# Performance work log

Measured on AMD Instinct MI355X. Metric: run time of the kernel, lower is better.

## Reference

```python
import jax, jax.numpy as jnp
import numpy as np
from jax import lax

B, C_IN, OUT_C, FEAT, W, HEADS, EXP = 2, 3, 12, 1024, 512, 4, 4
HEAD_DIM = FEAT // HEADS
EPS = 1e-8


def _u(key, shape, bound):
    return jax.random.uniform(key, shape, jnp.float32, -bound, bound)


def setup_inputs():
    key = jax.random.key(0)
    ks = jax.random.split(key, 16)
    fb = 1.0 / np.sqrt(FEAT)
    return {
        'x': jax.random.normal(ks[0], (B, C_IN, FEAT, W), jnp.float32),
        'embed_w': _u(ks[1], (OUT_C, C_IN, 1, 1), 1.0 / np.sqrt(C_IN)),
        'embed_b': _u(ks[2], (OUT_C,), 1.0 / np.sqrt(C_IN)),
        'ln1_w': jnp.ones((OUT_C, 1, FEAT), jnp.float32),
        'ln1_b': jnp.zeros((OUT_C, 1, FEAT), jnp.float32),
        'q_dw': _u(ks[3], (OUT_C, 1, 9, 9), 1.0 / 9.0),
        'q_pw': _u(ks[4], (OUT_C, FEAT, FEAT), fb),
        'k_dw': _u(ks[5], (OUT_C, 1, 9, 9), 1.0 / 9.0),
        'k_pw': _u(ks[6], (OUT_C, FEAT, FEAT), fb),
        'v_dw': _u(ks[7], (OUT_C, 1, 9, 9), 1.0 / 9.0),
        'v_pw': _u(ks[8], (OUT_C, FEAT, FEAT), fb),
        'o_pw': _u(ks[9], (OUT_C, FEAT, FEAT), fb),
        'ln2_w': jnp.ones((OUT_C, 1, FEAT), jnp.float32),
        'ln2_b': jnp.zeros((OUT_C, 1, FEAT), jnp.float32),
        'c1_w': _u(ks[10], (OUT_C * EXP, OUT_C, 3, 3), 1.0 / np.sqrt(OUT_C * 9)),
        'c1_b': _u(ks[11], (OUT_C * EXP,), 1.0 / np.sqrt(OUT_C * 9)),
        'c2_w': _u(ks[12], (OUT_C, OUT_C * EXP, 3, 3), 1.0 / np.sqrt(OUT_C * EXP * 9)),
        'c2_b': _u(ks[13], (OUT_C,), 1.0 / np.sqrt(OUT_C * EXP * 9)),
    }


def conv2d(x, w, b=None, pad=1, groups=1):
    y = lax.conv_general_dilated(x, w, (1, 1), [(pad, pad), (pad, pad)],
                                 dimension_numbers=('NCHW', 'OIHW', 'NCHW'),
                                 feature_group_count=groups)
    if b is not None:
        y = y + b[None, :, None, None]
    return y


def mc_layernorm(x, w, b):
    # LayerNorm over the feature (H) axis, per-channel affine. x: (b,c,h,w)
    xt = jnp.swapaxes(x, 2, 3)  # b,c,w,h
    mu = xt.mean(-1, keepdims=True)
    var = xt.var(-1, keepdims=True)
    y = (xt - mu) / jnp.sqrt(var + EPS) * w[:, 0, :][None, :, None, :] + b[:, 0, :][None, :, None, :]
    return jnp.swapaxes(y, 2, 3)


def mc_linear(x, w_pw):
    # per-channel linear over feature axis. x: (b,c,h,w), w_pw: (c,out_f,in_f)
    return jnp.einsum('bchw,cfh->bcfw', x, w_pw)


def rope(x):
    # interleaved rotary along the frame axis. x: (b,c,heads,w,d)
    d = x.shape[-1]
    inv = 1.0 / (10000.0 ** (jnp.arange(0, d, 2, dtype=jnp.float32) / d))
    t = jnp.arange(x.shape[-2], dtype=jnp.float32)
    freqs = jnp.repeat(t[:, None] * inv[None, :], 2, axis=-1)  # (w, d)
    cos, sin = jnp.cos(freqs), jnp.sin(freqs)
    xp = x.reshape(x.shape[:-1] + (d // 2, 2))
    xr = jnp.stack([-xp[..., 1], xp[..., 0]], -1).reshape(x.shape)
    return x * cos + xr * sin


def attention(x, q_dw, q_pw, k_dw, k_pw, v_dw, v_pw, o_pw):
    b, c, h, w = x.shape

    def proj(dw, pw):
        y = mc_linear(conv2d(x, dw, pad=4, groups=c), pw)  # b,c,h,w
        return jnp.swapaxes(y, 2, 3).reshape(b, c, w, HEADS, HEAD_DIM).transpose(0, 1, 3, 2, 4)

    q = rope(proj(q_dw, q_pw))
    k = rope(proj(k_dw, k_pw))
    v = proj(v_dw, v_pw)
    # NOTE: original scales by sqrt(h) = sqrt(features), not sqrt(head_dim)
    qk = jnp.einsum('bcnqd,bcnkd->bcnqk', q, k) / jnp.sqrt(jnp.float32(h))
    a = jnp.einsum('bcnqk,bcnkd->bcnqd', jax.nn.softmax(qk, -1), v)
    a = a.transpose(0, 1, 3, 2, 4).reshape(b, c, w, h)
    a = jnp.swapaxes(a, 2, 3)  # b,c,h,w
    return mc_linear(a, o_pw), qk


def _forward(x, embed_w, embed_b, ln1_w, ln1_b, q_dw, q_pw, k_dw, k_pw, v_dw, v_pw,
             o_pw, ln2_w, ln2_b, c1_w, c1_b, c2_w, c2_b):
    h = conv2d(x, embed_w, embed_b, pad=0)
    z, qk = attention(mc_layernorm(h, ln1_w, ln1_b), q_dw, q_pw, k_dw, k_pw, v_dw, v_pw, o_pw)
    h = h + z
    t = conv2d(mc_layernorm(h, ln2_w, ln2_b), c1_w, c1_b, pad=1)
    t = jnp.square(jax.nn.relu(t))
    z = conv2d(t, c2_w, c2_b, pad=1)
    h = h + z
    return jnp.concatenate((x, h), axis=1), h, qk


def reference(x, embed_w, embed_b, ln1_w, ln1_b, q_dw, q_pw, k_dw, k_pw, v_dw, v_pw,
              o_pw, ln2_w, ln2_b, c1_w, c1_b, c2_w, c2_b):
    return _forward(x, embed_w, embed_b, ln1_w, ln1_b, q_dw, q_pw, k_dw, k_pw, v_dw,
                    v_pw, o_pw, ln2_w, ln2_b, c1_w, c1_b, c2_w, c2_b)
```

## Files before the change

kernel.cpp:

```cpp
#include <hip/hip_runtime.h>
#include <math.h>

static constexpr int FEAT = 1024;
static constexpr int WDIM = 512;
static constexpr size_t PL = (size_t)FEAT * WDIM;
static constexpr size_t NB = (size_t)2 * 12 * PL;
static constexpr size_t HS = NB / 2;

typedef __attribute__((ext_vector_type(8))) short bf8_t;
typedef __attribute__((ext_vector_type(4))) float f4_t;

__device__ __forceinline__ ushort f2b(float f) {
  union { float f; unsigned u; } x; x.f = f;
  unsigned u = x.u;
  return (ushort)((u + 0x7FFFu + ((u >> 16) & 1u)) >> 16);
}

#define GLL16(g, l) __builtin_amdgcn_global_load_lds(                         \
    (const __attribute__((address_space(1))) void*)(g),                       \
    (__attribute__((address_space(3))) void*)(l), 16, 0, 0)

__global__ __launch_bounds__(256)
void k_embed(const float* __restrict__ x, const float* __restrict__ ew,
             const float* __restrict__ eb, float* __restrict__ h0)
{
  int t = blockIdx.x * 256 + threadIdx.x;
  int x4 = (t & 127) * 4;
  int y  = (t >> 7) & 1023;
  int b  = t >> 17;
  float4 xi0 = *(const float4*)&x[(((size_t)b*3+0)*FEAT + y)*WDIM + x4];
  float4 xi1 = *(const float4*)&x[(((size_t)b*3+1)*FEAT + y)*WDIM + x4];
  float4 xi2 = *(const float4*)&x[(((size_t)b*3+2)*FEAT + y)*WDIM + x4];
  #pragma unroll
  for (int c = 0; c < 12; c++) {
    float w0 = ew[c*3], w1 = ew[c*3+1], w2 = ew[c*3+2], bb = eb[c];
    float4 o;
    o.x = fmaf(xi0.x, w0, fmaf(xi1.x, w1, fmaf(xi2.x, w2, bb)));
    o.y = fmaf(xi0.y, w0, fmaf(xi1.y, w1, fmaf(xi2.y, w2, bb)));
    o.z = fmaf(xi0.z, w0, fmaf(xi1.z, w1, fmaf(xi2.z, w2, bb)));
    o.w = fmaf(xi0.w, w0, fmaf(xi1.w, w1, fmaf(xi2.w, w2, bb)));
    *(float4*)&h0[(((size_t)b*12+c)*FEAT + y)*WDIM + x4] = o;
  }
}

__global__ __launch_bounds__(256)
void k_ln(const float* __restrict__ in, const float* __restrict__ w,
          const float* __restrict__ bia, float* __restrict__ out)
{
  int bc = blockIdx.y; int c = bc % 12;
  int w0 = blockIdx.x * 64;
  int tx = threadIdx.x & 63, ty = threadIdx.x >> 6;
  const float* base = in + (size_t)bc*PL + w0;
  float s = 0.f, ss = 0.f;
  for (int h = ty; h < FEAT; h += 4) {
    float v = base[(size_t)h*WDIM + tx];
    s += v; ss = fmaf(v, v, ss);
  }
  __shared__ float S1[4][64], S2[4][64];
  S1[ty][tx] = s; S2[ty][tx] = ss;
  __syncthreads();
  if (ty == 0) {
    float t1 = S1[0][tx]+S1[1][tx]+S1[2][tx]+S1[3][tx];
    float t2 = S2[0][tx]+S2[1][tx]+S2[2][tx]+S2[3][tx];
    float mu = t1 * (1.0f/1024.0f);
    float var = t2 * (1.0f/1024.0f) - mu*mu;
    S1[0][tx] = mu; S2[0][tx] = rsqrtf(var + 1e-8f);
  }
  __syncthreads();
  float mu = S1[0][tx], ri = S2[0][tx];
  float* ob = out + (size_t)bc*PL + w0;
  for (int h = ty; h < FEAT; h += 4) {
    float v = base[(size_t)h*WDIM + tx];
    ob[(size_t)h*WDIM + tx] = (v - mu) * ri * w[c*FEAT + h] + bia[c*FEAT + h];
  }
}

__global__ __launch_bounds__(256)
void k_ln_b(const float* __restrict__ in, const float* __restrict__ w,
            const float* __restrict__ bia, ushort* __restrict__ out)
{
  int bc = blockIdx.y; int c = bc % 12;
  int w0 = blockIdx.x * 64;
  int tx = threadIdx.x & 63, ty = threadIdx.x >> 6;
  const float* base = in + (size_t)bc*PL + w0;
  float s = 0.f, ss = 0.f;
  for (int h = ty; h < FEAT; h += 4) {
    float v = base[(size_t)h*WDIM + tx];
    s += v; ss = fmaf(v, v, ss);
  }
  __shared__ float S1[4][64], S2[4][64];
  S1[ty][tx] = s; S2[ty][tx] = ss;
  __syncthreads();
  if (ty == 0) {
    float t1 = S1[0][tx]+S1[1][tx]+S1[2][tx]+S1[3][tx];
    float t2 = S2[0][tx]+S2[1][tx]+S2[2][tx]+S2[3][tx];
    float mu = t1 * (1.0f/1024.0f);
    float var = t2 * (1.0f/1024.0f) - mu*mu;
    S1[0][tx] = mu; S2[0][tx] = rsqrtf(var + 1e-8f);
  }
  __syncthreads();
  float mu = S1[0][tx], ri = S2[0][tx];
  ushort* ob = out + (size_t)bc*PL + w0;
  for (int h = ty; h < FEAT; h += 4) {
    float v = base[(size_t)h*WDIM + tx];
    ob[(size_t)h*WDIM + tx] = f2b((v - mu) * ri * w[c*FEAT + h] + bia[c*FEAT + h]);
  }
}

__global__ __launch_bounds__(256)
void k_dw3(const float* __restrict__ in, const float* __restrict__ wq,
           const float* __restrict__ wk, const float* __restrict__ wv,
           float* __restrict__ oq, float* __restrict__ ok, float* __restrict__ ov)
{
  __shared__ float tile[12][72];
  __shared__ float wsq[81], wsk[81], wsv[81];
  int bc = blockIdx.z; int c = bc % 12;
  int y0 = blockIdx.y * 4, w0 = blockIdx.x * 64;
  int tid = threadIdx.x;
  const float* base = in + (size_t)bc*PL;
  for (int idx = tid; idx < 12*72; idx += 256) {
    int hh = idx / 72, ww = idx % 72;
    int gh = y0 + hh - 4, gw = w0 + ww - 4;
    float v = 0.f;
    if (gh >= 0 && gh < 1024 && gw >= 0 && gw < 512) v = base[(size_t)gh*WDIM + gw];
    tile[hh][ww] = v;
  }
  if (tid < 81) { wsq[tid] = wq[c*81+tid]; wsk[tid] = wk[c*81+tid]; wsv[tid] = wv[c*81+tid]; }
  __syncthreads();
  int tx = tid & 63, ty = tid >> 6;
  float aq = 0.f, ak = 0.f, av = 0.f;
  #pragma unroll
  for (int dy = 0; dy < 9; dy++)
    #pragma unroll
    for (int dx = 0; dx < 9; dx++) {
      float v = tile[ty+dy][tx+dx];
      aq = fmaf(v, wsq[dy*9+dx], aq);
      ak = fmaf(v, wsk[dy*9+dx], ak);
      av = fmaf(v, wsv[dy*9+dx], av);
    }
  size_t o = (size_t)bc*PL + (size_t)(y0+ty)*WDIM + (w0+tx);
  oq[o] = aq; ok[o] = ak; ov[o] = av;
}

__global__ __launch_bounds__(256)
void k_tr3(const float* __restrict__ iq, const float* __restrict__ ik,
           const float* __restrict__ iv, ushort* __restrict__ oq,
           ushort* __restrict__ ok, ushort* __restrict__ ov)
{
  __shared__ float t[64][65];
  int bc = blockIdx.z; int h0 = blockIdx.y * 64, w0 = blockIdx.x * 64;
  size_t ib = (size_t)bc * PL;
  const float* ins[3] = {iq + ib, ik + ib, iv + ib};
  ushort* outs[3] = {oq + ib, ok + ib, ov + ib};
  #pragma unroll
  for (int a = 0; a < 3; a++) {
    if (a) __syncthreads();
    for (int i = threadIdx.x; i < 4096; i += 256) {
      int hh = i >> 6, ww = i & 63;
      t[hh][ww] = ins[a][(size_t)(h0+hh)*512 + w0 + ww];
    }
    __syncthreads();
    for (int i = threadIdx.x; i < 4096; i += 256) {
      int ww = i >> 6, hh = i & 63;
      outs[a][(size_t)(w0+ww)*1024 + h0 + hh] = f2b(t[hh][ww]);
    }
  }
}

__global__ __launch_bounds__(256)
void k_cvt(const float* __restrict__ in, ushort* __restrict__ out)
{
  size_t i = ((size_t)blockIdx.x * 256 + threadIdx.x) * 8;
  float4 v0 = *(const float4*)&in[i];
  float4 v1 = *(const float4*)&in[i+4];
  union { ushort u[8]; uint4 v; } o;
  o.u[0]=f2b(v0.x); o.u[1]=f2b(v0.y); o.u[2]=f2b(v0.z); o.u[3]=f2b(v0.w);
  o.u[4]=f2b(v1.x); o.u[5]=f2b(v1.y); o.u[6]=f2b(v1.z); o.u[7]=f2b(v1.w);
  *(uint4*)&out[i] = o.v;
}

__global__ __launch_bounds__(256)
void k_softmax(const float* __restrict__ qk, ushort* __restrict__ probs)
{
  int wave = threadIdx.x >> 6, lane = threadIdx.x & 63;
  size_t row = (size_t)blockIdx.x * 4 + wave;
  const float* r = qk + row * 512;
  float v[8];
  float m = -1e30f;
  #pragma unroll
  for (int j = 0; j < 8; j++) { v[j] = r[lane + 64*j]; m = fmaxf(m, v[j]); }
  #pragma unroll
  for (int o = 32; o; o >>= 1) m = fmaxf(m, __shfl_xor(m, o));
  float s = 0.f;
  #pragma unroll
  for (int j = 0; j < 8; j++) { v[j] = expf(v[j] - m); s += v[j]; }
  #pragma unroll
  for (int o = 32; o; o >>= 1) s += __shfl_xor(s, o);
  float inv = 1.0f / s;
  ushort* p = probs + row * 512;
  #pragma unroll
  for (int j = 0; j < 8; j++) p[lane + 64*j] = f2b(v[j] * inv);
}

template<int MODE>
__global__ __launch_bounds__(256)
void mgemm(const ushort* __restrict__ Ab, const ushort* __restrict__ Bb,
           void* __restrict__ Cb)
{
  constexpr int K   = (MODE==1) ? 256 : ((MODE==2) ? 512 : 1024);
  constexpr int LDA = (MODE==1) ? 256 : ((MODE==2) ? 512 : 1024);
  constexpr int LDB = LDA;

  const int z = blockIdx.z;
  const ushort* A; const ushort* B;
  if constexpr (MODE==0 || MODE==4) {
    int bc = z >> 2, head = z & 3, c = bc % 12;
    A = Ab + ((size_t)c*1024 + head*256)*1024;
    B = Bb + (size_t)bc*524288;
  } else if constexpr (MODE==1) {
    A = Ab + (size_t)z*131072; B = Bb + (size_t)z*131072;
  } else if constexpr (MODE==2) {
    A = Ab + (size_t)z*262144; B = Bb + (size_t)z*131072;
  } else {
    int c = z % 12;
    A = Ab + (size_t)c*1048576;
    B = Bb + (size_t)z*524288;
  }

  const int m0 = blockIdx.y * 128, n0 = blockIdx.x * 128;
  const int tid = threadIdx.x, lane = tid & 63, wv = tid >> 6;
  const int wr = wv >> 1, wc = wv & 1;
  const int lm = lane & 15, lg = lane >> 4;

  __shared__ __align__(16) ushort Alds[4096];
  __shared__ __align__(16) ushort Blds[4096];

  const ushort* gA0 = A + (size_t)(m0 + (2*wv)*16 + lm)*LDA + 8*lg;
  const ushort* gA1 = gA0 + (size_t)16*LDA;
  const ushort* gB0 = B + (size_t)(n0 + (2*wv)*16 + lm)*LDB + 8*lg;
  const ushort* gB1 = gB0 + (size_t)16*LDB;
  ushort* lA0 = &Alds[(2*wv)*512]; ushort* lA1 = lA0 + 512;
  ushort* lB0 = &Blds[(2*wv)*512]; ushort* lB1 = lB0 + 512;

  f4_t acc[4][4];
  #pragma unroll
  for (int i = 0; i < 4; i++)
    #pragma unroll
    for (int j = 0; j < 4; j++) acc[i][j] = (f4_t){0.f, 0.f, 0.f, 0.f};

  for (int k0 = 0; k0 < K; k0 += 32) {
    GLL16(gA0 + k0, lA0); GLL16(gA1 + k0, lA1);
    GLL16(gB0 + k0, lB0); GLL16(gB1 + k0, lB1);
    __syncthreads();
    bf8_t fa[4], fb[4];
    #pragma unroll
    for (int i = 0; i < 4; i++) fa[i] = *(const bf8_t*)&Alds[(wr*4+i)*512 + lane*8];
    #pragma unroll
    for (int j = 0; j < 4; j++) fb[j] = *(const bf8_t*)&Blds[(wc*4+j)*512 + lane*8];
    #pragma unroll
    for (int i = 0; i < 4; i++)
      #pragma unroll
      for (int j = 0; j < 4; j++)
        acc[i][j] = __builtin_amdgcn_mfma_f32_16x16x32_bf16(fa[i], fb[j], acc[i][j], 0, 0, 0);
    __syncthreads();
  }

  if constexpr (MODE==0) {
    ushort* C = (ushort*)Cb + (size_t)z*131072;
    #pragma unroll
    for (int j = 0; j < 4; j++) {
      int w = n0 + wc*64 + j*16 + lm;
      #pragma unroll
      for (int i = 0; i < 4; i++) {
        int d0 = m0 + wr*64 + i*16 + lg*4;
        int p0 = d0 >> 1;
        float inv0 = expf(-(float)p0 * 0.07195578432833848f);
        float inv1 = inv0 * 0.9305720409297794f;
        float s0, c0, s1, c1;
        sincosf((float)w * inv0, &s0, &c0);
        sincosf((float)w * inv1, &s1, &c1);
        f4_t a = acc[i][j];
        ushort4 o;
        o.x = f2b(a.x*c0 - a.y*s0);
        o.y = f2b(a.y*c0 + a.x*s0);
        o.z = f2b(a.z*c1 - a.w*s1);
        o.w = f2b(a.w*c1 + a.z*s1);
        *(ushort4*)&C[(size_t)w*256 + d0] = o;
      }
    }
  } else if constexpr (MODE==4) {
    ushort* C = (ushort*)Cb + (size_t)z*131072;
    #pragma unroll
    for (int i = 0; i < 4; i++) {
      int d0 = m0 + wr*64 + i*16 + lg*4;
      #pragma unroll
      for (int j = 0; j < 4; j++) {
        int w = n0 + wc*64 + j*16 + lm;
        f4_t a = acc[i][j];
        C[(size_t)(d0+0)*512 + w] = f2b(a.x);
        C[(size_t)(d0+1)*512 + w] = f2b(a.y);
        C[(size_t)(d0+2)*512 + w] = f2b(a.z);
        C[(size_t)(d0+3)*512 + w] = f2b(a.w);
      }
    }
  } else if constexpr (MODE==1) {
    float* C = (float*)Cb + (size_t)z*262144;
    #pragma unroll
    for (int i = 0; i < 4; i++) {
      int q0 = m0 + wr*64 + i*16 + lg*4;
      #pragma unroll
      for (int j = 0; j < 4; j++) {
        int kc = n0 + wc*64 + j*16 + lm;
        f4_t a = acc[i][j];
        C[(size_t)(q0+0)*512 + kc] = a.x * 0.03125f;
        C[(size_t)(q0+1)*512 + kc] = a.y * 0.03125f;
        C[(size_t)(q0+2)*512 + kc] = a.z * 0.03125f;
        C[(size_t)(q0+3)*512 + kc] = a.w * 0.03125f;
      }
    }
  } else if constexpr (MODE==2) {
    ushort* C = (ushort*)Cb + (size_t)(z>>2)*524288 + (size_t)(z&3)*256;
    #pragma unroll
    for (int i = 0; i < 4; i++) {
      int q0 = m0 + wr*64 + i*16 + lg*4;
      #pragma unroll
      for (int j = 0; j < 4; j++) {
        int d = n0 + wc*64 + j*16 + lm;
        f4_t a = acc[i][j];
        C[(size_t)(q0+0)*1024 + d] = f2b(a.x);
        C[(size_t)(q0+1)*1024 + d] = f2b(a.y);
        C[(size_t)(q0+2)*1024 + d] = f2b(a.z);
        C[(size_t)(q0+3)*1024 + d] = f2b(a.w);
      }
    }
  } else {
    float* C = (float*)Cb + (size_t)z*524288;
    #pragma unroll
    for (int i = 0; i < 4; i++) {
      int f0 = m0 + wr*64 + i*16 + lg*4;
      #pragma unroll
      for (int j = 0; j < 4; j++) {
        int w = n0 + wc*64 + j*16 + lm;
        f4_t a = acc[i][j];
        C[(size_t)(f0+0)*512 + w] += a.x;
        C[(size_t)(f0+1)*512 + w] += a.y;
        C[(size_t)(f0+2)*512 + w] += a.z;
        C[(size_t)(f0+3)*512 + w] += a.w;
      }
    }
  }
}

__global__ __launch_bounds__(256)
void k_pack(const float* __restrict__ c1w, const float* __restrict__ c2w,
            ushort* __restrict__ wp1, ushort* __restrict__ wp2)
{
  int tid = threadIdx.x;
  for (int i = tid; i < 48*168; i += 256) {
    int oc = i / 168, k = i % 168;
    ushort v = 0;
    if (k < 160) {
      int ofs = k >> 4, ch = k & 15;
      if (ofs < 9 && ch < 12) v = f2b(c1w[(oc*12 + ch)*9 + ofs]);
    }
    wp1[i] = v;
  }
  for (int i = tid; i < 16*584; i += 256) {
    int oc = i / 584, k = i % 584;
    ushort v = 0;
    if (k < 576) {
      int ofs = k >> 6, ch = k & 63;
      if (oc < 12 && ch < 48) v = f2b(c2w[(oc*48 + ch)*9 + ofs]);
    }
    wp2[i] = v;
  }
}

__global__ __launch_bounds__(256)
void k_c1m(const ushort* __restrict__ in, const ushort* __restrict__ Wp,
           const float* __restrict__ bias, ushort* __restrict__ out)
{
  __shared__ __align__(16) ushort Wl[48*168];
  __shared__ __align__(16) ushort Xl[4*136*16];
  __shared__ float Bs[48];
  const int b = blockIdx.z, ybase = blockIdx.y*8, x0 = blockIdx.x*128;
  const int tid = threadIdx.x, lane = tid & 63, wv = tid >> 6;
  const int lm = lane & 15, lg = lane >> 4;
  const int hl = lg >> 1, cbs = lg & 1;

  for (int i = tid; i < 48*168; i += 256) Wl[i] = Wp[i];
  for (int i = tid; i < 4*136*16; i += 256) Xl[i] = 0;
  if (tid < 48) Bs[tid] = bias[tid];

  for (int y8 = 0; y8 < 8; y8++) {
    int y = ybase + y8;
    __syncthreads();
    for (int i = tid; i < 3*34*12; i += 256) {
      int ch = i % 12, cc = (i/12) % 34, r = i/(12*34);
      int sy = y + r - 1, sx = x0 - 4 + cc*4;
      ushort4 v = (ushort4){0,0,0,0};
      if ((unsigned)sy < 1024u) {
        const ushort* p = in + ((size_t)(b*12+ch)*1024 + sy)*512 + sx;
        if (sx >= 0 && sx <= 508) v = *(const ushort4*)p;
        else {
          ushort tv[4] = {0,0,0,0};
          #pragma unroll
          for (int u = 0; u < 4; u++) { int xx = sx+u; if ((unsigned)xx < 512u) tv[u] = p[u]; }
          v = (ushort4){tv[0],tv[1],tv[2],tv[3]};
        }
      }
      int cb = ch >> 3, ce = ch & 7;
      #pragma unroll
      for (int u = 0; u < 4; u++) {
        int col = cc*4 + u;
        Xl[((r*136 + col) << 4) + ((cb ^ (col & 1)) << 3) + ce] = ((const ushort*)&v)[u];
      }
    }
    __syncthreads();

    f4_t acc[3][2];
    #pragma unroll
    for (int i = 0; i < 3; i++) { acc[i][0] = (f4_t){0,0,0,0}; acc[i][1] = (f4_t){0,0,0,0}; }
    #pragma unroll
    for (int s = 0; s < 5; s++) {
      bf8_t af[3];
      #pragma unroll
      for (int mf = 0; mf < 3; mf++)
        af[mf] = *(const bf8_t*)&Wl[(mf*16 + lm)*168 + s*32 + lg*8];
      int ofs = 2*s + hl;
      int dy = ofs / 3, dx = ofs - dy*3;
      #pragma unroll
      for (int nf = 0; nf < 2; nf++) {
        int col = (wv*2 + nf)*16 + lm + dx + 3;
        bf8_t bf = *(const bf8_t*)&Xl[((dy*136 + col) << 4) + ((cbs ^ (col & 1)) << 3)];
        #pragma unroll
        for (int mf = 0; mf < 3; mf++)
          acc[mf][nf] = __builtin_amdgcn_mfma_f32_16x16x32_bf16(af[mf], bf, acc[mf][nf], 0, 0, 0);
      }
    }
    #pragma unroll
    for (int nf = 0; nf < 2; nf++) {
      int p = (wv*2 + nf)*16 + lm;
      ushort* op = out + (((size_t)(b*1024 + y)*512) + x0 + p)*48;
      #pragma unroll
      for (int mf = 0; mf < 3; mf++) {
        int oc0 = mf*16 + lg*4;
        f4_t a = acc[mf][nf];
        float r0 = fmaxf(a.x + Bs[oc0+0], 0.f);
        float r1 = fmaxf(a.y + Bs[oc0+1], 0.f);
        float r2 = fmaxf(a.z + Bs[oc0+2], 0.f);
        float r3 = fmaxf(a.w + Bs[oc0+3], 0.f);
        ushort4 o;
        o.x = f2b(r0*r0); o.y = f2b(r1*r1); o.z = f2b(r2*r2); o.w = f2b(r3*r3);
        *(ushort4*)&op[oc0] = o;
      }
    }
  }
}

__global__ __launch_bounds__(256)
void k_c2m(const ushort* __restrict__ tin, const ushort* __restrict__ Wp,
           const float* __restrict__ bias, const float* __restrict__ h1,
           float* __restrict__ out0, float* __restrict__ out1)
{
  __shared__ __align__(16) ushort Wl[16*584];
  __shared__ __align__(16) ushort Xl[3*132*64];
  __shared__ float Bs[12];
  const int b = blockIdx.z, ybase = blockIdx.y*8, x0 = blockIdx.x*128;
  const int tid = threadIdx.x, lane = tid & 63, wv = tid >> 6;
  const int lm = lane & 15, lg = lane >> 4;

  for (int i = tid; i < 16*584; i += 256) Wl[i] = Wp[i];
  for (int i = tid; i < 3*132*64; i += 256) Xl[i] = 0;
  if (tid < 12) Bs[tid] = bias[tid];

  for (int y8 = 0; y8 < 8; y8++) {
    int y = ybase + y8;
    __syncthreads();
    for (int i = tid; i < 3*132*6; i += 256) {
      int ck = i % 6, col = (i/6) % 132, r = i/(6*132);
      int sy = y + r - 1, sx = x0 + col - 1;
      uint4 v = (uint4){0u,0u,0u,0u};
      if ((unsigned)sy < 1024u && (unsigned)sx < 512u)
        v = *(const uint4*)&tin[(((size_t)(b*1024 + sy)*512 + sx)*48) + ck*8];
      *(uint4*)&Xl[((r*132 + col) << 6) + ((ck ^ (col & 7)) << 3)] = v;
    }
    __syncthreads();

    f4_t acc[2];
    acc[0] = (f4_t){0,0,0,0}; acc[1] = (f4_t){0,0,0,0};
    #pragma unroll
    for (int s = 0; s < 18; s++) {
      bf8_t af = *(const bf8_t*)&Wl[lm*584 + s*32 + lg*8];
      int ofs = s >> 1;
      int dy = ofs / 3, dx = ofs - dy*3;
      int cb = ((s & 1) << 2) + lg;
      #pragma unroll
      for (int nf = 0; nf < 2; nf++) {
        int col = (wv*2 + nf)*16 + lm + dx;
        bf8_t bf = *(const bf8_t*)&Xl[((dy*132 + col) << 6) + ((cb ^ (col & 7)) << 3)];
        acc[nf] = __builtin_amdgcn_mfma_f32_16x16x32_bf16(af, bf, acc[nf], 0, 0, 0);
      }
    }
    if (lg < 3) {
      #pragma unroll
      for (int nf = 0; nf < 2; nf++) {
        int p = x0 + (wv*2 + nf)*16 + lm;
        f4_t a = acc[nf];
        #pragma unroll
        for (int r = 0; r < 4; r++) {
          int oc = lg*4 + r;
          size_t po = ((size_t)(b*12 + oc)*1024 + y)*512 + p;
          float hv = a[r] + Bs[oc] + h1[po];
          out1[po] = hv;
          out0[((size_t)(b*15 + 3 + oc)*1024 + y)*512 + p] = hv;
        }
      }
    }
  }
}

__global__ __launch_bounds__(256)
void k_copyx(const float* __restrict__ x, float* __restrict__ out0)
{
  int t = blockIdx.x * 256 + threadIdx.x;
  int x4 = (t & 127) * 4;
  int y  = (t >> 7) & 1023;
  int ci = (t >> 17) % 3;
  int b  = t / 393216;
  *(float4*)&out0[(((size_t)b*15 + ci)*FEAT + y)*WDIM + x4] =
      *(const float4*)&x[(((size_t)b*3 + ci)*FEAT + y)*WDIM + x4];
}

extern "C" void kernel_launch(void* const* d_in, const int* in_sizes, int n_in,
                              void* d_out, int out_size, void* d_ws, size_t ws_size,
                              hipStream_t stream)
{
  const float* x       = (const float*)d_in[0];
  const float* embed_w = (const float*)d_in[1];
  const float* embed_b = (const float*)d_in[2];
  const float* ln1_w   = (const float*)d_in[3];
  const float* ln1_b   = (const float*)d_in[4];
  const float* q_dw    = (const float*)d_in[5];
  const float* q_pw    = (const float*)d_in[6];
  const float* k_dw    = (const float*)d_in[7];
  const float* k_pw    = (const float*)d_in[8];
  const float* v_dw    = (const float*)d_in[9];
  const float* v_pw    = (const float*)d_in[10];
  const float* o_pw    = (const float*)d_in[11];
  const float* ln2_w   = (const float*)d_in[12];
  const float* ln2_b   = (const float*)d_in[13];
  const float* c1_w    = (const float*)d_in[14];
  const float* c1_b    = (const float*)d_in[15];
  const float* c2_w    = (const float*)d_in[16];
  const float* c2_b    = (const float*)d_in[17];

  float* ws = (float*)d_ws;
  float*  h0   = ws + 0*HS;
  float*  lnb  = ws + 2*HS;
  float*  dwq  = ws + 4*HS;
  float*  dwk  = ws + 6*HS;
  float*  dwv  = ws + 8*HS;
  ushort* dwtq = (ushort*)(ws + 10*HS);
  ushort* dwtk = (ushort*)(ws + 11*HS);
  ushort* dwtv = (ushort*)(ws + 12*HS);
  ushort* pwbq = (ushort*)(ws + 4*HS);
  ushort* pwbk = (ushort*)(ws + 5*HS);
  ushort* pwbv = (ushort*)(ws + 6*HS);
  ushort* pwbo = (ushort*)(ws + 7*HS);
  ushort* Qb   = (ushort*)(ws + 8*HS);
  ushort* Kb   = (ushort*)(ws + 9*HS);
  ushort* Vb   = (ushort*)(ws + 13*HS);
  ushort* probs= (ushort*)(ws + 10*HS);
  ushort* attt = (ushort*)(ws + 12*HS);
  ushort* Wp1  = (ushort*)(ws + 4*HS);
  ushort* Wp2  = Wp1 + 48*168;
  ushort* lnb_b= (ushort*)(ws + 2*HS);
  ushort* tcl  = (ushort*)(ws + 8*HS);

  float* out0 = (float*)d_out;
  float* out1 = out0 + (size_t)2*15*FEAT*WDIM;
  float* qk   = out1 + NB;

  k_embed<<<1024, 256, 0, stream>>>(x, embed_w, embed_b, h0);
  k_ln<<<dim3(8, 24), 256, 0, stream>>>(h0, ln1_w, ln1_b, lnb);
  k_dw3<<<dim3(8, 256, 24), 256, 0, stream>>>(lnb, q_dw, k_dw, v_dw, dwq, dwk, dwv);
  k_tr3<<<dim3(8, 16, 24), 256, 0, stream>>>(dwq, dwk, dwv, dwtq, dwtk, dwtv);
  k_cvt<<<6144, 256, 0, stream>>>(q_pw, pwbq);
  k_cvt<<<6144, 256, 0, stream>>>(k_pw, pwbk);
  k_cvt<<<6144, 256, 0, stream>>>(v_pw, pwbv);
  k_cvt<<<6144, 256, 0, stream>>>(o_pw, pwbo);
  mgemm<0><<<dim3(4, 2, 96), 256, 0, stream>>>(pwbq, dwtq, Qb);
  mgemm<0><<<dim3(4, 2, 96), 256, 0, stream>>>(pwbk, dwtk, Kb);
  mgemm<4><<<dim3(4, 2, 96), 256, 0, stream>>>(pwbv, dwtv, Vb);
  mgemm<1><<<dim3(4, 4, 96), 256, 0, stream>>>(Qb, Kb, qk);
  k_softmax<<<12288, 256, 0, stream>>>(qk, probs);
  mgemm<2><<<dim3(2, 4, 96), 256, 0, stream>>>(probs, Vb, attt);
  mgemm<3><<<dim3(4, 8, 24), 256, 0, stream>>>(pwbo, attt, (void*)h0);
  k_pack<<<1, 256, 0, stream>>>(c1_w, c2_w, Wp1, Wp2);
  k_ln_b<<<dim3(8, 24), 256, 0, stream>>>(h0, ln2_w, ln2_b, lnb_b);
  k_c1m<<<dim3(4, 128, 2), 256, 0, stream>>>(lnb_b, Wp1, c1_b, tcl);
  k_c2m<<<dim3(4, 128, 2), 256, 0, stream>>>(tcl, Wp2, c2_b, h0, out0, out1);
  k_copyx<<<3072, 256, 0, stream>>>(x, out0);
}
```

Baseline: 1.337 ms.

## Fuse depthwise conv with transpose to bf16 and batch weight conversion and Q/K GEMMs

Merges the 9x9 depthwise conv and the transpose/bf16 conversion into one kernel that computes 64x64 tiles with register blocking and writes transposed bf16 output through LDS. This removes the fp32 intermediate round trip. The four weight conversions become one launch, and the Q and K projection GEMMs run as a single launch over a doubled grid. Workspace offsets are reshuffled so the Q/K buffers sit NB apart. This adds register pressure from 48 accumulators and is fragile to buffer aliasing.

```diff
diff --git a/kernel.cpp b/kernel.cpp
--- a/kernel.cpp
+++ b/kernel.cpp
@@ -108,75 +108,95 @@
 }
 
 __global__ __launch_bounds__(256)
-void k_dw3(const float* __restrict__ in, const float* __restrict__ wq,
-           const float* __restrict__ wk, const float* __restrict__ wv,
-           float* __restrict__ oq, float* __restrict__ ok, float* __restrict__ ov)
-{
-  __shared__ float tile[12][72];
-  __shared__ float wsq[81], wsk[81], wsv[81];
-  int bc = blockIdx.z; int c = bc % 12;
-  int y0 = blockIdx.y * 4, w0 = blockIdx.x * 64;
-  int tid = threadIdx.x;
+void k_dw3t(const float* __restrict__ in, const float* __restrict__ wq,
+            const float* __restrict__ wk, const float* __restrict__ wvv,
+            ushort* __restrict__ oq, ushort* __restrict__ ok2, ushort* __restrict__ ov)
+{
+  __shared__ float tile[72*72];
+  __shared__ float wsm[3][81];
+  const int bc = blockIdx.z, c = bc % 12;
+  const int y0 = blockIdx.y * 64, x0 = blockIdx.x * 64;
+  const int tid = threadIdx.x, lane = tid & 63, wv_ = tid >> 6;
   const float* base = in + (size_t)bc*PL;
-  for (int idx = tid; idx < 12*72; idx += 256) {
-    int hh = idx / 72, ww = idx % 72;
-    int gh = y0 + hh - 4, gw = w0 + ww - 4;
-    float v = 0.f;
-    if (gh >= 0 && gh < 1024 && gw >= 0 && gw < 512) v = base[(size_t)gh*WDIM + gw];
-    tile[hh][ww] = v;
-  }
-  if (tid < 81) { wsq[tid] = wq[c*81+tid]; wsk[tid] = wk[c*81+tid]; wsv[tid] = wv[c*81+tid]; }
+
+  for (int i = tid; i < 1296; i += 256) {
+    int r = i / 18, c4 = (i % 18) * 4;
+    int gy = y0 - 4 + r, gx = x0 - 4 + c4;
+    float4 v = {0.f,0.f,0.f,0.f};
+    if ((unsigned)gy < 1024u && (unsigned)gx < 512u)
+      v = *(const float4*)&base[(size_t)gy*512 + gx];
+    *(float4*)&tile[r*72 + c4] = v;
+  }
+  if (tid < 81) { wsm[0][tid] = wq[c*81+tid]; wsm[1][tid] = wk[c*81+tid]; wsm[2][tid] = wvv[c*81+tid]; }
   __syncthreads();
-  int tx = tid & 63, ty = tid >> 6;
-  float aq = 0.f, ak = 0.f, av = 0.f;
-  #pragma unroll
-  for (int dy = 0; dy < 9; dy++)
-    #pragma unroll
-    for (int dx = 0; dx < 9; dx++) {
-      float v = tile[ty+dy][tx+dx];
-      aq = fmaf(v, wsq[dy*9+dx], aq);
-      ak = fmaf(v, wsk[dy*9+dx], ak);
-      av = fmaf(v, wsv[dy*9+dx], av);
-    }
-  size_t o = (size_t)bc*PL + (size_t)(y0+ty)*WDIM + (w0+tx);
-  oq[o] = aq; ok[o] = ak; ov[o] = av;
-}
-
-__global__ __launch_bounds__(256)
-void k_tr3(const float* __restrict__ iq, const float* __restrict__ ik,
-           const float* __restrict__ iv, ushort* __restrict__ oq,
-           ushort* __restrict__ ok, ushort* __restrict__ ov)
-{
-  __shared__ float t[64][65];
-  int bc = blockIdx.z; int h0 = blockIdx.y * 64, w0 = blockIdx.x * 64;
-  size_t ib = (size_t)bc * PL;
-  const float* ins[3] = {iq + ib, ik + ib, iv + ib};
-  ushort* outs[3] = {oq + ib, ok + ib, ov + ib};
-  #pragma unroll
-  for (int a = 0; a < 3; a++) {
-    if (a) __syncthreads();
-    for (int i = threadIdx.x; i < 4096; i += 256) {
-      int hh = i >> 6, ww = i & 63;
-      t[hh][ww] = ins[a][(size_t)(h0+hh)*512 + w0 + ww];
-    }
-    __syncthreads();
-    for (int i = threadIdx.x; i < 4096; i += 256) {
-      int ww = i >> 6, hh = i & 63;
-      outs[a][(size_t)(w0+ww)*1024 + h0 + hh] = f2b(t[hh][ww]);
-    }
-  }
-}
-
-__global__ __launch_bounds__(256)
-void k_cvt(const float* __restrict__ in, ushort* __restrict__ out)
-{
+
+  float aq[16] = {}, ak[16] = {}, av[16] = {};
+  #pragma unroll 1
+  for (int dx = 0; dx < 9; dx++) {
+    float wq9[9], wk9[9], wv9[9];
+    #pragma unroll
+    for (int dy = 0; dy < 9; dy++) {
+      wq9[dy] = wsm[0][dy*9+dx]; wk9[dy] = wsm[1][dy*9+dx]; wv9[dy] = wsm[2][dy*9+dx];
+    }
+    const float* col = &tile[(wv_*16)*72 + lane + dx];
+    #pragma unroll
+    for (int r = 0; r < 24; r++) {
+      float v = col[r*72];
+      int dylo = (r > 15) ? (r - 15) : 0;
+      int dyhi = (r < 8) ? r : 8;
+      #pragma unroll
+      for (int dy = 0; dy < 9; dy++) {
+        if (dy >= dylo && dy <= dyhi) {
+          aq[r-dy] = fmaf(v, wq9[dy], aq[r-dy]);
+          ak[r-dy] = fmaf(v, wk9[dy], ak[r-dy]);
+          av[r-dy] = fmaf(v, wv9[dy], av[r-dy]);
+        }
+      }
+    }
+  }
+
+  ushort* T = (ushort*)tile;
+#define DW_EMIT(ACC, OUT)                                                     \
+  {                                                                           \
+    __syncthreads();                                                          \
+    uint pk[8];                                                               \
+    _Pragma("unroll")                                                         \
+    for (int u = 0; u < 8; u++)                                               \
+      pk[u] = (uint)f2b(ACC[2*u]) | ((uint)f2b(ACC[2*u+1]) << 16);            \
+    uint4* dst = (uint4*)&T[lane*72 + wv_*16];                                \
+    dst[0] = make_uint4(pk[0],pk[1],pk[2],pk[3]);                             \
+    dst[1] = make_uint4(pk[4],pk[5],pk[6],pk[7]);                             \
+    __syncthreads();                                                          \
+    ushort* op = OUT + (size_t)bc*PL;                                         \
+    _Pragma("unroll")                                                         \
+    for (int it = 0; it < 2; it++) {                                          \
+      int idx = it*256 + tid;                                                 \
+      int xr = idx >> 3, y8 = (idx & 7) * 8;                                  \
+      uint4 vv = *(uint4*)&T[xr*72 + y8];                                     \
+      *(uint4*)&op[(size_t)(x0+xr)*1024 + y0 + y8] = vv;                      \
+    }                                                                         \
+  }
+  DW_EMIT(aq, oq)
+  DW_EMIT(ak, ok2)
+  DW_EMIT(av, ov)
+#undef DW_EMIT
+}
+
+__global__ __launch_bounds__(256)
+void k_cvt4(const float* __restrict__ p0, const float* __restrict__ p1,
+            const float* __restrict__ p2, const float* __restrict__ p3,
+            ushort* __restrict__ out)
+{
+  const float* ins[4] = {p0, p1, p2, p3};
+  const float* in = ins[blockIdx.y];
   size_t i = ((size_t)blockIdx.x * 256 + threadIdx.x) * 8;
+  ushort* o = out + (size_t)blockIdx.y * NB + i;
   float4 v0 = *(const float4*)&in[i];
   float4 v1 = *(const float4*)&in[i+4];
-  union { ushort u[8]; uint4 v; } o;
-  o.u[0]=f2b(v0.x); o.u[1]=f2b(v0.y); o.u[2]=f2b(v0.z); o.u[3]=f2b(v0.w);
-  o.u[4]=f2b(v1.x); o.u[5]=f2b(v1.y); o.u[6]=f2b(v1.z); o.u[7]=f2b(v1.w);
-  *(uint4*)&out[i] = o.v;
+  union { ushort u[8]; uint4 v; } t;
+  t.u[0]=f2b(v0.x); t.u[1]=f2b(v0.y); t.u[2]=f2b(v0.z); t.u[3]=f2b(v0.w);
+  t.u[4]=f2b(v1.x); t.u[5]=f2b(v1.y); t.u[6]=f2b(v1.z); t.u[7]=f2b(v1.w);
+  *(uint4*)o = t.v;
 }
 
 __global__ __launch_bounds__(256)
@@ -213,10 +233,12 @@
 
   const int z = blockIdx.z;
   const ushort* A; const ushort* B;
+  int zz = z; size_t toff = 0;
   if constexpr (MODE==0 || MODE==4) {
-    int bc = z >> 2, head = z & 3, c = bc % 12;
-    A = Ab + ((size_t)c*1024 + head*256)*1024;
-    B = Bb + (size_t)bc*524288;
+    if constexpr (MODE==0) { int t = (z >= 96); zz = z - 96*t; toff = (size_t)t * NB; }
+    int bc = zz >> 2, head = zz & 3, c = bc % 12;
+    A = Ab + toff + ((size_t)c*1024 + head*256)*1024;
+    B = Bb + toff + (size_t)bc*524288;
   } else if constexpr (MODE==1) {
     A = Ab + (size_t)z*131072; B = Bb + (size_t)z*131072;
   } else if constexpr (MODE==2) {
@@ -266,7 +288,7 @@
   }
 
   if constexpr (MODE==0) {
-    ushort* C = (ushort*)Cb + (size_t)z*131072;
+    ushort* C = (ushort*)Cb + toff + (size_t)zz*131072;
     #pragma unroll
     for (int j = 0; j < 4; j++) {
       int w = n0 + wc*64 + j*16 + lm;
@@ -558,25 +580,19 @@
   float* ws = (float*)d_ws;
   float*  h0   = ws + 0*HS;
   float*  lnb  = ws + 2*HS;
-  float*  dwq  = ws + 4*HS;
-  float*  dwk  = ws + 6*HS;
-  float*  dwv  = ws + 8*HS;
-  ushort* dwtq = (ushort*)(ws + 10*HS);
-  ushort* dwtk = (ushort*)(ws + 11*HS);
-  ushort* dwtv = (ushort*)(ws + 12*HS);
-  ushort* pwbq = (ushort*)(ws + 4*HS);
-  ushort* pwbk = (ushort*)(ws + 5*HS);
-  ushort* pwbv = (ushort*)(ws + 6*HS);
-  ushort* pwbo = (ushort*)(ws + 7*HS);
-  ushort* Qb   = (ushort*)(ws + 8*HS);
-  ushort* Kb   = (ushort*)(ws + 9*HS);
+  ushort* dwtq = (ushort*)(ws + 4*HS);
+  ushort* dwtk = (ushort*)(ws + 5*HS);
+  ushort* dwtv = (ushort*)(ws + 6*HS);
+  ushort* pwbq = (ushort*)(ws + 7*HS);
+  ushort* pwbo = (ushort*)(ws + 10*HS);
+  ushort* Qb   = (ushort*)(ws + 11*HS);
   ushort* Vb   = (ushort*)(ws + 13*HS);
-  ushort* probs= (ushort*)(ws + 10*HS);
-  ushort* attt = (ushort*)(ws + 12*HS);
+  ushort* probs= (ushort*)(ws + 4*HS);
+  ushort* attt = (ushort*)(ws + 6*HS);
   ushort* Wp1  = (ushort*)(ws + 4*HS);
   ushort* Wp2  = Wp1 + 48*168;
   ushort* lnb_b= (ushort*)(ws + 2*HS);
-  ushort* tcl  = (ushort*)(ws + 8*HS);
+  ushort* tcl  = (ushort*)(ws + 7*HS);
 
   float* out0 = (float*)d_out;
   float* out1 = out0 + (size_t)2*15*FEAT*WDIM;
@@ -584,16 +600,11 @@
 
   k_embed<<<1024, 256, 0, stream>>>(x, embed_w, embed_b, h0);
   k_ln<<<dim3(8, 24), 256, 0, stream>>>(h0, ln1_w, ln1_b, lnb);
-  k_dw3<<<dim3(8, 256, 24), 256, 0, stream>>>(lnb, q_dw, k_dw, v_dw, dwq, dwk, dwv);
-  k_tr3<<<dim3(8, 16, 24), 256, 0, stream>>>(dwq, dwk, dwv, dwtq, dwtk, dwtv);
-  k_cvt<<<6144, 256, 0, stream>>>(q_pw, pwbq);
-  k_cvt<<<6144, 256, 0, stream>>>(k_pw, pwbk);
-  k_cvt<<<6144, 256, 0, stream>>>(v_pw, pwbv);
-  k_cvt<<<6144, 256, 0, stream>>>(o_pw, pwbo);
-  mgemm<0><<<dim3(4, 2, 96), 256, 0, stream>>>(pwbq, dwtq, Qb);
-  mgemm<0><<<dim3(4, 2, 96), 256, 0, stream>>>(pwbk, dwtk, Kb);
-  mgemm<4><<<dim3(4, 2, 96), 256, 0, stream>>>(pwbv, dwtv, Vb);
-  mgemm<1><<<dim3(4, 4, 96), 256, 0, stream>>>(Qb, Kb, qk);
+  k_dw3t<<<dim3(8, 16, 24), 256, 0, stream>>>(lnb, q_dw, k_dw, v_dw, dwtq, dwtk, dwtv);
+  k_cvt4<<<dim3(6144, 4), 256, 0, stream>>>(q_pw, k_pw, v_pw, o_pw, pwbq);
+  mgemm<0><<<dim3(4, 2, 192), 256, 0, stream>>>(pwbq, dwtq, Qb);
+  mgemm<4><<<dim3(4, 2, 96), 256, 0, stream>>>((ushort*)(ws + 9*HS), dwtv, Vb);
+  mgemm<1><<<dim3(4, 4, 96), 256, 0, stream>>>(Qb, (ushort*)(ws + 12*HS), qk);
   k_softmax<<<12288, 256, 0, stream>>>(qk, probs);
   mgemm<2><<<dim3(2, 4, 96), 256, 0, stream>>>(probs, Vb, attt);
   mgemm<3><<<dim3(4, 8, 24), 256, 0, stream>>>(pwbo, attt, (void*)h0);
```

Measured after the change: 1.199 ms. 1.11x faster.
